# Optimization experiments

Measured on AMD Instinct MI355X. Metric: run time of the kernel, lower is better.

Reference implementation:

```python
import jax, jax.numpy as jnp
import numpy as np
from jax.ops import segment_sum, segment_max

N_NODES, N_EDGES, N_GRAPHS = 50000, 800000, 128
IN_C, HID, HEADS, CLIN = 64, 64, 4, 32


def gat_layer(x, W, a_s, a_d, b, src, dst, n):
    # GAT-style attention conv with concatenated heads (PyG GATConv math).
    H, C = a_s.shape
    h = (x @ W).reshape(-1, H, C)                      # [N,H,C]
    es = jnp.einsum('nhc,hc->nh', h, a_s)
    ed = jnp.einsum('nhc,hc->nh', h, a_d)
    e = jax.nn.leaky_relu(es[src] + ed[dst], 0.2)      # [E,H]
    m = segment_max(e, dst, num_segments=n)            # stable softmax over incoming edges
    e = jnp.exp(e - m[dst])
    denom = segment_sum(e, dst, num_segments=n)
    alpha = e / jnp.where(denom[dst] > 0, denom[dst], 1.0)
    out = segment_sum(h[src] * alpha[:, :, None], dst, num_segments=n)  # [N,H,C]
    return out.reshape(-1, H * C) + b


def label_prop(x, src, dst, n, num_layers=2, alpha=0.5):
    # PyG LabelPropagation: sym-normalized diffusion, residual mix, clamp to [0,1].
    deg = segment_sum(jnp.ones((src.shape[0],), x.dtype), dst, num_segments=n)
    dis = jnp.where(deg > 0, 1.0 / jnp.sqrt(jnp.maximum(deg, 1.0)), 0.0)
    norm = (dis[src] * dis[dst])[:, None]
    res = (1.0 - alpha) * x
    out = x
    for _ in range(num_layers):
        out = alpha * segment_sum(out[src] * norm, dst, num_segments=n) + res
        out = jnp.clip(out, 0.0, 1.0)
    return out


def mean_pool(x, batch, n_graphs):
    cnt = segment_sum(jnp.ones((x.shape[0],), x.dtype), batch, num_segments=n_graphs)
    s = segment_sum(x, batch, num_segments=n_graphs)
    return s / jnp.maximum(cnt, 1.0)[:, None]


def setup_inputs() -> dict:
    key = jax.random.key(0)
    ks = iter(jax.random.split(key, 32))
    def p(shape, fan_in):
        return jax.random.normal(next(ks), shape, jnp.float32) / np.sqrt(fan_in)
    d = {}
    d['x'] = jax.random.normal(next(ks), (N_NODES, IN_C), jnp.float32)
    d['edge_index'] = jax.random.randint(next(ks), (2, N_EDGES), 0, N_NODES)
    d['batch'] = jnp.sort(jax.random.randint(next(ks), (N_NODES,), 0, N_GRAPHS))
    d['clinical_data'] = jax.random.normal(next(ks), (N_GRAPHS, CLIN), jnp.float32)
    HC = HEADS * HID
    d['W1'] = p((IN_C, HC), IN_C); d['a1s'] = p((HEADS, HID), HID); d['a1d'] = p((HEADS, HID), HID); d['b1'] = jnp.zeros((HC,), jnp.float32)
    d['W2'] = p((HC, HC), HC); d['a2s'] = p((HEADS, HID), HID); d['a2d'] = p((HEADS, HID), HID); d['b2'] = jnp.zeros((HC,), jnp.float32)
    jk = IN_C + 2 * HC  # 576
    d['pp_w1'] = p((jk, 256), jk); d['pp_b1'] = jnp.zeros((256,), jnp.float32)
    d['pp_w2'] = p((256, 128), 256); d['pp_b2'] = jnp.zeros((128,), jnp.float32)
    d['cl_w1'] = p((CLIN, 64), CLIN); d['cl_b1'] = jnp.zeros((64,), jnp.float32)
    d['cl_w2'] = p((64, 32), 64); d['cl_b2'] = jnp.zeros((32,), jnp.float32)
    d['h_w1'] = p((160, 64), 160); d['h_b1'] = jnp.zeros((64,), jnp.float32)
    d['h_w2'] = p((64, 32), 64); d['h_b2'] = jnp.zeros((32,), jnp.float32)
    d['h_w3'] = p((32, 2), 32); d['h_b3'] = jnp.zeros((2,), jnp.float32)
    return d


def reference(x, edge_index, batch, clinical_data,
              W1, a1s, a1d, b1, W2, a2s, a2d, b2,
              pp_w1, pp_b1, pp_w2, pp_b2,
              cl_w1, cl_b1, cl_w2, cl_b2,
              h_w1, h_b1, h_w2, h_b2, h_w3, h_b3):
    src, dst = edge_index[0], edge_index[1]
    n = x.shape[0]
    h0 = x
    h1 = jax.nn.relu(gat_layer(h0, W1, a1s, a1d, b1, src, dst, n))
    h1 = label_prop(h1, src, dst, n)
    h2 = jax.nn.relu(gat_layer(h1, W2, a2s, a2d, b2, src, dst, n))
    h2 = label_prop(h2, src, dst, n)
    combined = jnp.concatenate([h0, h1, h2], axis=-1)           # [N, 576]
    g = mean_pool(combined, batch, N_GRAPHS)                    # [G, 576]
    v_graph = jax.nn.relu(g @ pp_w1 + pp_b1) @ pp_w2 + pp_b2    # [G, 128] (dropout = eval/no-op)
    v_clin = jax.nn.relu(clinical_data @ cl_w1 + cl_b1) @ cl_w2 + cl_b2  # [G, 32]
    z = jnp.concatenate([v_graph, v_clin], axis=-1)             # [G, 160]
    z = jax.nn.relu(z @ h_w1 + h_b1)
    z = jax.nn.relu(z @ h_w2 + h_b2)
    return z @ h_w3 + h_b3                                      # [G, 2]
```

## Files before the change

kernel.cpp:

```cpp
#include <hip/hip_runtime.h>

#define N_NODES 50000
#define N_EDGES 800000
#define N_GRAPHS 128
#define JK 576
#define CAP 192
#define NSB ((N_NODES + 255) / 256)
#define SLICE_U (N_NODES * 16)

typedef __attribute__((ext_vector_type(8))) short bf16x8;
typedef __attribute__((ext_vector_type(4))) float f32x4;

__device__ __forceinline__ unsigned f2_to_bf2(float a, float b) {
    unsigned ua = __float_as_uint(a), ub = __float_as_uint(b);
    ua = (ua + 0x7fffu + ((ua >> 16) & 1u)) >> 16;
    ub = (ub + 0x7fffu + ((ub >> 16) & 1u)) >> 16;
    return ua | (ub << 16);
}
__device__ __forceinline__ uint2 f4_to_bf4(float4 v) {
    return make_uint2(f2_to_bf2(v.x, v.y), f2_to_bf2(v.z, v.w));
}
__device__ __forceinline__ float4 bf4_to_f4(uint2 u) {
    float4 r;
    r.x = __uint_as_float(u.x << 16);
    r.y = __uint_as_float(u.x & 0xffff0000u);
    r.z = __uint_as_float(u.y << 16);
    r.w = __uint_as_float(u.y & 0xffff0000u);
    return r;
}

template<int BN, int KK, int SLA, int SLC>
__global__ __launch_bounds__(256)
void mfma_gemm(const unsigned short* __restrict__ Abf, int lda,
               const unsigned short* __restrict__ BT,
               unsigned* __restrict__ Cbf, int ldc,
               int M, const float* __restrict__ bias, int relu,
               int a_off, int b_off, int c_off) {
    __shared__ unsigned short As[64][32];
    __shared__ unsigned short Bs[BN][32];
    const int t = threadIdx.x;
    const int wav = t >> 6, lane = t & 63;
    const int quad = lane >> 4, l15 = lane & 15;
    const int m0 = blockIdx.x * 64;
    const int head = blockIdx.y;
    const unsigned short* Ab = Abf + (size_t)head * a_off;
    BT  += (size_t)head * b_off;
    const float* bptr = bias ? bias + (size_t)head * c_off : nullptr;
    unsigned* cbf = Cbf + (((size_t)head * c_off) >> 1);

    f32x4 acc[BN / 16];
#pragma unroll
    for (int i = 0; i < BN / 16; i++) acc[i] = (f32x4){0.f, 0.f, 0.f, 0.f};

    const int arow = t >> 2, aseg = t & 3;
    for (int k0 = 0; k0 < KK; k0 += 32) {
        uint4 av = make_uint4(0, 0, 0, 0);
        int gm = m0 + arow;
        if (gm < M) {
            if (SLA) {
                av = *(const uint4*)&Ab[(size_t)(k0 >> 5) * (N_NODES * 32) +
                                        (size_t)gm * 32 + aseg * 8];
            } else {
                av = *(const uint4*)&Ab[(size_t)gm * lda + k0 + aseg * 8];
            }
        }
        uint4 bv[BN == 256 ? 4 : 1];
        if (BN == 256) {
            const unsigned short* srcb = &BT[(size_t)t * KK + k0];
#pragma unroll
            for (int j = 0; j < 4; j++) bv[j] = *(const uint4*)&srcb[j * 8];
        } else {
            bv[0] = *(const uint4*)&BT[(size_t)arow * KK + k0 + aseg * 8];
        }
        __syncthreads();
        *(uint4*)&As[arow][aseg * 8] = av;
        if (BN == 256) {
#pragma unroll
            for (int j = 0; j < 4; j++) *(uint4*)&Bs[t][j * 8] = bv[j];
        } else {
            *(uint4*)&Bs[arow][aseg * 8] = bv[0];
        }
        __syncthreads();
        bf16x8 afrag = *(const bf16x8*)&As[wav * 16 + l15][quad * 8];
#pragma unroll
        for (int nt = 0; nt < BN / 16; nt++) {
            bf16x8 bfrag = *(const bf16x8*)&Bs[nt * 16 + l15][quad * 8];
            acc[nt] = __builtin_amdgcn_mfma_f32_16x16x32_bf16(afrag, bfrag, acc[nt], 0, 0, 0);
        }
    }
    int rbase = m0 + wav * 16 + quad * 4;
#pragma unroll
    for (int nt = 0; nt < BN / 16; nt++) {
        int col = nt * 16 + l15;
        float bb = bptr ? bptr[col] : 0.f;
#pragma unroll
        for (int r = 0; r < 4; r++) {
            int row = rbase + r;
            float v = acc[nt][r] + bb;
            if (relu) v = fmaxf(v, 0.f);
            float vp = __shfl_xor(v, 1);
            if (row < M && !(l15 & 1)) {
                if (SLC) {
                    int ch = head * c_off + col;
                    size_t a = (size_t)(ch >> 5) * SLICE_U + (size_t)row * 16 + ((ch & 31) >> 1);
                    Cbf[a] = f2_to_bf2(v, vp);
                } else {
                    cbf[((size_t)row * ldc + col) >> 1] = f2_to_bf2(v, vp);
                }
            }
        }
    }
}

__global__ void deg_kernel(const int* __restrict__ dst, int* __restrict__ deg,
                           const int* __restrict__ batch, int* __restrict__ gstart) {
    int t = blockIdx.x * blockDim.x + threadIdx.x;
    if (t < N_EDGES) {
        atomicAdd(&deg[dst[t]], 1);
    } else if (t < N_EDGES + N_NODES) {
        int n = t - N_EDGES;
        int b = batch[n];
        int prev = (n == 0) ? -1 : batch[n - 1];
        for (int g = prev + 1; g <= b; g++) gstart[g] = n;
        if (n == N_NODES - 1)
            for (int g = b + 1; g <= N_GRAPHS; g++) gstart[g] = N_NODES;
    }
}

#define S1 50000
#define S2 50256
#define S3 51280
#define S4 67664
#define S5 133200
#define S6 1733200
#define S7 (S6 + 131072)
__global__ void prep_misc(const int* __restrict__ deg, float* __restrict__ dis,
                          const float* __restrict__ W1, const float* __restrict__ a1s,
                          const float* __restrict__ a1d, float* __restrict__ wes1,
                          float* __restrict__ wed1,
                          const float* __restrict__ W2, const float* __restrict__ a2s,
                          const float* __restrict__ a2d, float* __restrict__ wes2,
                          float* __restrict__ wed2,
                          unsigned short* __restrict__ W1T, unsigned short* __restrict__ W2T,
                          const float* __restrict__ x, unsigned* __restrict__ xbf,
                          const int* __restrict__ gstart, float* __restrict__ psum) {
    int i = blockIdx.x * blockDim.x + threadIdx.x;
    if (i >= S7) return;
    if (i >= S6) {
        int t2 = i - S6;
        int g = t2 >> 10, rem = t2 & 1023;
        int q = rem >> 8, tid = rem & 255;
        int cp = tid & 63, np = tid >> 6;
        int n0 = gstart[g], n1 = gstart[g + 1];
        int len = n1 - n0;
        int ns = n0 + (len * q) / 4, ne = n0 + (len * (q + 1)) / 4;
        float s = 0.f;
        for (int n = ns + np; n < ne; n += 4) s += x[(size_t)n * 64 + cp];
        atomicAdd(&psum[g * JK + cp], s);
    } else if (i >= S5) {
        int j = i - S5;
        float2 v = *(const float2*)&x[(size_t)j * 2];
        xbf[j] = f2_to_bf2(v.x, v.y);
    } else if (i >= S4) {
        int t2 = i - S4;
        int n = t2 >> 8, c = t2 & 255;
        unsigned u = __float_as_uint(W2[(size_t)c * 256 + n]);
        u = (u + 0x7fffu + ((u >> 16) & 1u)) >> 16;
        W2T[t2] = (unsigned short)u;
    } else if (i >= S3) {
        int t2 = i - S3;
        int n = t2 >> 6, c = t2 & 63;
        unsigned u = __float_as_uint(W1[(size_t)c * 256 + n]);
        u = (u + 0x7fffu + ((u >> 16) & 1u)) >> 16;
        W1T[t2] = (unsigned short)u;
    } else if (i >= S2) {
        int t2 = i - S2;
        int c = t2 >> 2, h = t2 & 3;
        float se = 0.f, sd = 0.f;
        for (int j = 0; j < 64; j++) {
            float w = W2[(size_t)c * 256 + h * 64 + j];
            se += w * a2s[h * 64 + j];
            sd += w * a2d[h * 64 + j];
        }
        wes2[c * 4 + h] = se;
        wed2[c * 4 + h] = sd;
    } else if (i >= S1) {
        int t2 = i - S1;
        int c = t2 >> 2, h = t2 & 3;
        float se = 0.f, sd = 0.f;
        for (int j = 0; j < 64; j++) {
            float w = W1[(size_t)c * 256 + h * 64 + j];
            se += w * a1s[h * 64 + j];
            sd += w * a1d[h * 64 + j];
        }
        wes1[c * 4 + h] = se;
        wed1[c * 4 + h] = sd;
    } else {
        int d = deg[i];
        dis[i] = d > 0 ? rsqrtf((float)d) : 0.f;
    }
}
__global__ __launch_bounds__(256) void scan_bsum(const int* __restrict__ deg,
                                                 int* __restrict__ bsum) {
    __shared__ int sd[256];
    int n = blockIdx.x * 256 + threadIdx.x;
    sd[threadIdx.x] = (n < N_NODES) ? deg[n] : 0;
    __syncthreads();
    for (int o = 128; o > 0; o >>= 1) {
        if (threadIdx.x < o) sd[threadIdx.x] += sd[threadIdx.x + o];
        __syncthreads();
    }
    if (threadIdx.x == 0) bsum[blockIdx.x] = sd[0];
}
__global__ __launch_bounds__(256) void scan_bpre(const int* __restrict__ bsum,
                                                 int* __restrict__ bpre,
                                                 int* __restrict__ off_last) {
    __shared__ int sd[256];
    int t = threadIdx.x;
    int v = (t < NSB) ? bsum[t] : 0;
    sd[t] = v;
    __syncthreads();
    for (int o = 1; o < 256; o <<= 1) {
        int u = (t >= o) ? sd[t - o] : 0;
        __syncthreads();
        sd[t] += u;
        __syncthreads();
    }
    if (t < NSB) bpre[t] = sd[t] - v;
    if (t == 255) *off_last = sd[255];
}
__global__ __launch_bounds__(256) void scan_off(const int* __restrict__ deg,
                                                const int* __restrict__ bpre,
                                                int* __restrict__ off) {
    __shared__ int sd[256];
    int n = blockIdx.x * 256 + threadIdx.x;
    int t = threadIdx.x;
    int v = (n < N_NODES) ? deg[n] : 0;
    sd[t] = v;
    __syncthreads();
    for (int o = 1; o < 256; o <<= 1) {
        int u = (t >= o) ? sd[t - o] : 0;
        __syncthreads();
        sd[t] += u;
        __syncthreads();
    }
    if (n < N_NODES) off[n] = bpre[blockIdx.x] + sd[t] - v;
}
__global__ void csr_fill(const int* __restrict__ src, const int* __restrict__ dst,
                         const int* __restrict__ off, int* __restrict__ cursor,
                         int* __restrict__ csr_src, int2* __restrict__ csr_sw,
                         const float* __restrict__ dis) {
    int e = blockIdx.x * blockDim.x + threadIdx.x;
    if (e == 0) csr_sw[N_EDGES] = make_int2(0, 0);
    if (e >= N_EDGES) return;
    int s = src[e], d = dst[e];
    int pos = off[d] + atomicAdd(&cursor[d], 1);
    csr_src[pos] = s;
    float w = dis[s] * dis[d];
    csr_sw[pos] = make_int2(s, __float_as_int(w));
}

__global__ void esed_x(const float* __restrict__ X, const float* __restrict__ wes,
                       const float* __restrict__ wed, float* __restrict__ es,
                       float* __restrict__ ed) {
    int gid = blockIdx.x * blockDim.x + threadIdx.x;
    int n = gid >> 6, lane = threadIdx.x & 63;
    if (n >= N_NODES) return;
    float xv = X[(size_t)n * 64 + lane];
    float4 a = *(const float4*)&wes[lane * 4];
    float4 b = *(const float4*)&wed[lane * 4];
    float4 ps = make_float4(xv * a.x, xv * a.y, xv * a.z, xv * a.w);
    float4 pd = make_float4(xv * b.x, xv * b.y, xv * b.z, xv * b.w);
#pragma unroll
    for (int o = 1; o < 64; o <<= 1) {
        ps.x += __shfl_xor(ps.x, o); ps.y += __shfl_xor(ps.y, o);
        ps.z += __shfl_xor(ps.z, o); ps.w += __shfl_xor(ps.w, o);
        pd.x += __shfl_xor(pd.x, o); pd.y += __shfl_xor(pd.y, o);
        pd.z += __shfl_xor(pd.z, o); pd.w += __shfl_xor(pd.w, o);
    }
    if (lane == 0) {
        *(float4*)&es[n * 4] = ps;
        *(float4*)&ed[n * 4] = pd;
    }
}

__global__ void esed_h(const unsigned* __restrict__ Hsl, const float* __restrict__ wes,
                       const float* __restrict__ wed, float* __restrict__ es,
                       float* __restrict__ ed) {
    int gid = blockIdx.x * blockDim.x + threadIdx.x;
    int n = gid >> 6, lane = threadIdx.x & 63;
    if (n >= N_NODES) return;
    int sl = lane >> 3;
    uint2 u = *(const uint2*)&Hsl[(size_t)sl * SLICE_U + (size_t)n * 16 + (lane & 7) * 2];
    float4 vv = bf4_to_f4(u);
    float v0 = vv.x, v1 = vv.y, v2 = vv.z, v3 = vv.w;
    int ch0 = lane * 4;
    float4 a0 = *(const float4*)&wes[(ch0 + 0) * 4];
    float4 a1 = *(const float4*)&wes[(ch0 + 1) * 4];
    float4 a2 = *(const float4*)&wes[(ch0 + 2) * 4];
    float4 a3 = *(const float4*)&wes[(ch0 + 3) * 4];
    float4 b0 = *(const float4*)&wed[(ch0 + 0) * 4];
    float4 b1 = *(const float4*)&wed[(ch0 + 1) * 4];
    float4 b2 = *(const float4*)&wed[(ch0 + 2) * 4];
    float4 b3 = *(const float4*)&wed[(ch0 + 3) * 4];
    float4 ps, pd;
    ps.x = v0 * a0.x + v1 * a1.x + v2 * a2.x + v3 * a3.x;
    ps.y = v0 * a0.y + v1 * a1.y + v2 * a2.y + v3 * a3.y;
    ps.z = v0 * a0.z + v1 * a1.z + v2 * a2.z + v3 * a3.z;
    ps.w = v0 * a0.w + v1 * a1.w + v2 * a2.w + v3 * a3.w;
    pd.x = v0 * b0.x + v1 * b1.x + v2 * b2.x + v3 * b3.x;
    pd.y = v0 * b0.y + v1 * b1.y + v2 * b2.y + v3 * b3.y;
    pd.z = v0 * b0.z + v1 * b1.z + v2 * b2.z + v3 * b3.z;
    pd.w = v0 * b0.w + v1 * b1.w + v2 * b2.w + v3 * b3.w;
#pragma unroll
    for (int o = 1; o < 64; o <<= 1) {
        ps.x += __shfl_xor(ps.x, o); ps.y += __shfl_xor(ps.y, o);
        ps.z += __shfl_xor(ps.z, o); ps.w += __shfl_xor(ps.w, o);
        pd.x += __shfl_xor(pd.x, o); pd.y += __shfl_xor(pd.y, o);
        pd.z += __shfl_xor(pd.z, o); pd.w += __shfl_xor(pd.w, o);
    }
    if (lane == 0) {
        *(float4*)&es[n * 4] = ps;
        *(float4*)&ed[n * 4] = pd;
    }
}

__global__ __launch_bounds__(256)
void gat1_fused(const int* __restrict__ off, const int* __restrict__ csr_src,
                const float* __restrict__ es, const float* __restrict__ ed,
                const unsigned* __restrict__ xbf, unsigned* __restrict__ aggx_bf,
                float* __restrict__ alpha_fb) {
    __shared__ float elds[4][CAP * 4];
    __shared__ int   sidx[4][CAP];
    int wav = threadIdx.x >> 6, lane = threadIdx.x & 63;
    int n = blockIdx.x * 4 + wav;
    bool active = n < N_NODES;
    int p0 = 0, p1 = 0;
    float4 ed4 = make_float4(0.f, 0.f, 0.f, 0.f);
    if (active) { p0 = off[n]; p1 = off[n + 1]; ed4 = *(const float4*)&ed[n * 4]; }
    float4 sum = make_float4(0.f, 0.f, 0.f, 0.f);
    for (int p = p0 + lane; p < p1; p += 64) {
        int s = csr_src[p];
        float4 e4 = *(const float4*)&es[s * 4];
        e4.x += ed4.x; e4.y += ed4.y; e4.z += ed4.z; e4.w += ed4.w;
        e4.x = e4.x > 0.f ? e4.x : 0.2f * e4.x;
        e4.y = e4.y > 0.f ? e4.y : 0.2f * e4.y;
        e4.z = e4.z > 0.f ? e4.z : 0.2f * e4.z;
        e4.w = e4.w > 0.f ? e4.w : 0.2f * e4.w;
        e4.x = __expf(e4.x); e4.y = __expf(e4.y); e4.z = __expf(e4.z); e4.w = __expf(e4.w);
        int q = p - p0;
        if (q < CAP) { *(float4*)&elds[wav][q * 4] = e4; sidx[wav][q] = s; }
        else         *(float4*)&alpha_fb[(size_t)p * 4] = e4;
        sum.x += e4.x; sum.y += e4.y; sum.z += e4.z; sum.w += e4.w;
    }
#pragma unroll
    for (int o = 1; o < 64; o <<= 1) {
        sum.x += __shfl_xor(sum.x, o); sum.y += __shfl_xor(sum.y, o);
        sum.z += __shfl_xor(sum.z, o); sum.w += __shfl_xor(sum.w, o);
    }
    float4 rs;
    rs.x = sum.x > 0.f ? 1.f / sum.x : 0.f;
    rs.y = sum.y > 0.f ? 1.f / sum.y : 0.f;
    rs.z = sum.z > 0.f ? 1.f / sum.z : 0.f;
    rs.w = sum.w > 0.f ? 1.f / sum.w : 0.f;
    if (!active) return;
    int eg = lane >> 4, l15 = lane & 15;
    int deg = p1 - p0;
    float4 a0 = make_float4(0.f, 0.f, 0.f, 0.f);
    float4 a1 = a0, a2 = a0, a3 = a0;
    auto fetch = [&](int qq, float4& e4, float4& xv) {
        e4 = make_float4(0.f, 0.f, 0.f, 0.f);
        xv = e4;
        if (qq < deg) {
            int s;
            if (qq < CAP) { s = sidx[wav][qq]; e4 = *(const float4*)&elds[wav][qq * 4]; }
            else { s = csr_src[p0 + qq]; e4 = *(const float4*)&alpha_fb[(size_t)(p0 + qq) * 4]; }
            xv = bf4_to_f4(*(const uint2*)&xbf[(size_t)s * 32 + l15 * 2]);
        }
    };
    int q = eg;
    float4 eA, xA, eB, xB, eC, xC;
    fetch(q, eA, xA);
    fetch(q + 4, eB, xB);
    fetch(q + 8, eC, xC);
    while (q < deg) {
        float4 eD, xD;
        fetch(q + 12, eD, xD);
        a0.x += eA.x * xA.x; a0.y += eA.x * xA.y; a0.z += eA.x * xA.z; a0.w += eA.x * xA.w;
        a1.x += eA.y * xA.x; a1.y += eA.y * xA.y; a1.z += eA.y * xA.z; a1.w += eA.y * xA.w;
        a2.x += eA.z * xA.x; a2.y += eA.z * xA.y; a2.z += eA.z * xA.z; a2.w += eA.z * xA.w;
        a3.x += eA.w * xA.x; a3.y += eA.w * xA.y; a3.z += eA.w * xA.z; a3.w += eA.w * xA.w;
        eA = eB; xA = xB; eB = eC; xB = xC; eC = eD; xC = xD;
        q += 4;
    }
#pragma unroll
    for (int o = 16; o < 64; o <<= 1) {
        a0.x += __shfl_xor(a0.x, o); a0.y += __shfl_xor(a0.y, o);
        a0.z += __shfl_xor(a0.z, o); a0.w += __shfl_xor(a0.w, o);
        a1.x += __shfl_xor(a1.x, o); a1.y += __shfl_xor(a1.y, o);
        a1.z += __shfl_xor(a1.z, o); a1.w += __shfl_xor(a1.w, o);
        a2.x += __shfl_xor(a2.x, o); a2.y += __shfl_xor(a2.y, o);
        a2.z += __shfl_xor(a2.z, o); a2.w += __shfl_xor(a2.w, o);
        a3.x += __shfl_xor(a3.x, o); a3.y += __shfl_xor(a3.y, o);
        a3.z += __shfl_xor(a3.z, o); a3.w += __shfl_xor(a3.w, o);
    }
    if (eg == 0) {
        a0.x *= rs.x; a0.y *= rs.x; a0.z *= rs.x; a0.w *= rs.x;
        a1.x *= rs.y; a1.y *= rs.y; a1.z *= rs.y; a1.w *= rs.y;
        a2.x *= rs.z; a2.y *= rs.z; a2.z *= rs.z; a2.w *= rs.z;
        a3.x *= rs.w; a3.y *= rs.w; a3.z *= rs.w; a3.w *= rs.w;
        size_t b = (size_t)n * 128 + l15 * 2;
        *(uint2*)&aggx_bf[b +  0] = f4_to_bf4(a0);
        *(uint2*)&aggx_bf[b + 32] = f4_to_bf4(a1);
        *(uint2*)&aggx_bf[b + 64] = f4_to_bf4(a2);
        *(uint2*)&aggx_bf[b + 96] = f4_to_bf4(a3);
    }
}

__global__ __launch_bounds__(256)
void gat2_fused(const int* __restrict__ off, const int* __restrict__ csr_src,
                const float* __restrict__ es, const float* __restrict__ ed,
                const unsigned* __restrict__ H2bf, const float* __restrict__ bias,
                unsigned* __restrict__ outbf, float* __restrict__ alpha_fb) {
    __shared__ float elds[4][CAP * 4];
    __shared__ int   sidx[4][CAP];
    int wav = threadIdx.x >> 6, lane = threadIdx.x & 63;
    int n = blockIdx.x * 4 + wav;
    bool active = n < N_NODES;
    int p0 = 0, p1 = 0;
    float4 ed4 = make_float4(0.f, 0.f, 0.f, 0.f);
    if (active) { p0 = off[n]; p1 = off[n + 1]; ed4 = *(const float4*)&ed[n * 4]; }
    float4 sum = make_float4(0.f, 0.f, 0.f, 0.f);
    for (int p = p0 + lane; p < p1; p += 64) {
        int s = csr_src[p];
        float4 e4 = *(const float4*)&es[s * 4];
        e4.x += ed4.x; e4.y += ed4.y; e4.z += ed4.z; e4.w += ed4.w;
        e4.x = e4.x > 0.f ? e4.x : 0.2f * e4.x;
        e4.y = e4.y > 0.f ? e4.y : 0.2f * e4.y;
        e4.z = e4.z > 0.f ? e4.z : 0.2f * e4.z;
        e4.w = e4.w > 0.f ? e4.w : 0.2f * e4.w;
        e4.x = __expf(e4.x); e4.y = __expf(e4.y); e4.z = __expf(e4.z); e4.w = __expf(e4.w);
        int q = p - p0;
        if (q < CAP) { *(float4*)&elds[wav][q * 4] = e4; sidx[wav][q] = s; }
        else         *(float4*)&alpha_fb[(size_t)p * 4] = e4;
        sum.x += e4.x; sum.y += e4.y; sum.z += e4.z; sum.w += e4.w;
    }
#pragma unroll
    for (int o = 1; o < 64; o <<= 1) {
        sum.x += __shfl_xor(sum.x, o); sum.y += __shfl_xor(sum.y, o);
        sum.z += __shfl_xor(sum.z, o); sum.w += __shfl_xor(sum.w, o);
    }
    if (!active) return;
    int half = lane >> 5, l = lane & 31;
    int hh = l >> 3;
    float sh = (hh == 0) ? sum.x : (hh == 1) ? sum.y : (hh == 2) ? sum.z : sum.w;
    float rsh = sh > 0.f ? 1.f / sh : 0.f;
    int deg = p1 - p0;
    float acc[8];
#pragma unroll
    for (int j = 0; j < 8; j++) acc[j] = 0.f;
    auto fetch = [&](int qq, float& al, uint4& rr) {
        al = 0.f;
        rr = make_uint4(0, 0, 0, 0);
        if (qq < deg) {
            int s;
            if (qq < CAP) { s = sidx[wav][qq]; al = elds[wav][qq * 4 + hh]; }
            else { s = csr_src[p0 + qq]; al = alpha_fb[(size_t)(p0 + qq) * 4 + hh]; }
            rr = *(const uint4*)&H2bf[(size_t)s * 128 + l * 4];
        }
    };
    int q = half;
    float aA, aB, aC;
    uint4 rA, rB, rC;
    fetch(q, aA, rA);
    fetch(q + 2, aB, rB);
    fetch(q + 4, aC, rC);
    while (q < deg) {
        float aD; uint4 rD;
        fetch(q + 6, aD, rD);
        float4 f0 = bf4_to_f4(make_uint2(rA.x, rA.y));
        float4 f1 = bf4_to_f4(make_uint2(rA.z, rA.w));
        acc[0] += aA * f0.x; acc[1] += aA * f0.y; acc[2] += aA * f0.z; acc[3] += aA * f0.w;
        acc[4] += aA * f1.x; acc[5] += aA * f1.y; acc[6] += aA * f1.z; acc[7] += aA * f1.w;
        aA = aB; rA = rB; aB = aC; rB = rC; aC = aD; rC = rD;
        q += 2;
    }
#pragma unroll
    for (int j = 0; j < 8; j++) acc[j] += __shfl_xor(acc[j], 32);
    if (half == 0) {
        float4 b0 = *(const float4*)&bias[l * 8];
        float4 b1 = *(const float4*)&bias[l * 8 + 4];
        float4 o0, o1;
        o0.x = fmaxf(acc[0] * rsh + b0.x, 0.f);
        o0.y = fmaxf(acc[1] * rsh + b0.y, 0.f);
        o0.z = fmaxf(acc[2] * rsh + b0.z, 0.f);
        o0.w = fmaxf(acc[3] * rsh + b0.w, 0.f);
        o1.x = fmaxf(acc[4] * rsh + b1.x, 0.f);
        o1.y = fmaxf(acc[5] * rsh + b1.y, 0.f);
        o1.z = fmaxf(acc[6] * rsh + b1.z, 0.f);
        o1.w = fmaxf(acc[7] * rsh + b1.w, 0.f);
        uint2 w0 = f4_to_bf4(o0), w1 = f4_to_bf4(o1);
        uint4 w = make_uint4(w0.x, w0.y, w1.x, w1.y);
        size_t a = (size_t)(l >> 2) * SLICE_U + (size_t)n * 16 + (l & 3) * 4;
        *(uint4*)&outbf[a] = w;
    }
}

__global__ __launch_bounds__(256)
void lp_slice(const int* __restrict__ off, const int2* __restrict__ csr_sw,
              const unsigned* __restrict__ in_sl,
              const unsigned* __restrict__ res_sl, unsigned* __restrict__ out_sl) {
    int wav = threadIdx.x >> 6, lane = threadIdx.x & 63;
    int sl = blockIdx.x & 7, chunk = blockIdx.x >> 3;
    int n0 = chunk * 16 + wav * 4;
    int nsub = lane >> 4, e = (lane >> 2) & 3, seg = lane & 3;
    int n = n0 + nsub;
    int p0 = 0, p1 = 0;
    if (n < N_NODES) { p0 = off[n]; p1 = off[n + 1]; }
    int m = (p1 - p0 + 3) >> 2;
    m = max(m, __shfl_xor(m, 16));
    m = max(m, __shfl_xor(m, 32));
    const unsigned* base = in_sl + (size_t)sl * SLICE_U;
    float acc[8];
#pragma unroll
    for (int j = 0; j < 8; j++) acc[j] = 0.f;
    int p = p0 + e;
    if (m > 0) {
        int pe = (p < p1) ? p : N_EDGES;
        int2 sw = csr_sw[pe];
        for (int i = 0; i < m; i++) {
            p += 4;
            int pen = (p < p1 && i + 1 < m) ? p : N_EDGES;
            int2 swn = csr_sw[pen];
            float nw = __int_as_float(sw.y);
            uint4 rr = *(const uint4*)&base[((unsigned)sw.x << 4) + (seg << 2)];
            float4 f0 = bf4_to_f4(make_uint2(rr.x, rr.y));
            float4 f1 = bf4_to_f4(make_uint2(rr.z, rr.w));
            acc[0] += nw * f0.x; acc[1] += nw * f0.y;
            acc[2] += nw * f0.z; acc[3] += nw * f0.w;
            acc[4] += nw * f1.x; acc[5] += nw * f1.y;
            acc[6] += nw * f1.z; acc[7] += nw * f1.w;
            sw = swn;
        }
    }
#pragma unroll
    for (int o = 4; o <= 8; o <<= 1) {
#pragma unroll
        for (int j = 0; j < 8; j++) acc[j] += __shfl_xor(acc[j], o);
    }
    if (((lane & 12) == 0) && n < N_NODES) {
        size_t a = (size_t)sl * SLICE_U + (size_t)n * 16 + (seg << 2);
        uint4 rr = *(const uint4*)&res_sl[a];
        float4 r0 = bf4_to_f4(make_uint2(rr.x, rr.y));
        float4 r1 = bf4_to_f4(make_uint2(rr.z, rr.w));
        float4 o0, o1;
        o0.x = fminf(fmaxf(0.5f * acc[0] + 0.5f * r0.x, 0.f), 1.f);
        o0.y = fminf(fmaxf(0.5f * acc[1] + 0.5f * r0.y, 0.f), 1.f);
        o0.z = fminf(fmaxf(0.5f * acc[2] + 0.5f * r0.z, 0.f), 1.f);
        o0.w = fminf(fmaxf(0.5f * acc[3] + 0.5f * r0.w, 0.f), 1.f);
        o1.x = fminf(fmaxf(0.5f * acc[4] + 0.5f * r1.x, 0.f), 1.f);
        o1.y = fminf(fmaxf(0.5f * acc[5] + 0.5f * r1.y, 0.f), 1.f);
        o1.z = fminf(fmaxf(0.5f * acc[6] + 0.5f * r1.z, 0.f), 1.f);
        o1.w = fminf(fmaxf(0.5f * acc[7] + 0.5f * r1.w, 0.f), 1.f);
        uint2 w0 = f4_to_bf4(o0), w1 = f4_to_bf4(o1);
        *(uint4*)&out_sl[a] = make_uint4(w0.x, w0.y, w1.x, w1.y);
    }
}

__global__ void pool_bf(const unsigned* __restrict__ buf, const int* __restrict__ gstart,
                        float* __restrict__ psum, int colOff) {
    int g = blockIdx.x, q = blockIdx.y;
    int n0 = gstart[g], n1 = gstart[g + 1];
    int len = n1 - n0;
    int ns = n0 + (len * q) / 4, ne = n0 + (len * (q + 1)) / 4;
    int cp = threadIdx.x & 127;
    int np = threadIdx.x >> 7;
    size_t sbase = (size_t)(cp >> 4) * SLICE_U + (cp & 15);
    float s0 = 0.f, s1 = 0.f;
    for (int n = ns + np; n < ne; n += 2) {
        unsigned u = buf[sbase + (size_t)n * 16];
        s0 += __uint_as_float(u << 16);
        s1 += __uint_as_float(u & 0xffff0000u);
    }
    atomicAdd(&psum[g * JK + colOff + cp * 2 + 0], s0);
    atomicAdd(&psum[g * JK + colOff + cp * 2 + 1], s1);
}

__global__ __launch_bounds__(256)
void head_all(const float* __restrict__ psum, const int* __restrict__ gstart,
              const float* __restrict__ clin,
              const float* __restrict__ pp_w1, const float* __restrict__ pp_b1,
              const float* __restrict__ pp_w2, const float* __restrict__ pp_b2,
              const float* __restrict__ cl_w1, const float* __restrict__ cl_b1,
              const float* __restrict__ cl_w2, const float* __restrict__ cl_b2,
              const float* __restrict__ h_w1, const float* __restrict__ h_b1,
              const float* __restrict__ h_w2, const float* __restrict__ h_b2,
              const float* __restrict__ h_w3, const float* __restrict__ h_b3,
              float* __restrict__ out) {
    __shared__ float zin[JK];
    __shared__ float z1[256];
    __shared__ float zcl[32];
    __shared__ float zc[64];
    __shared__ float z[160];
    __shared__ float z3[64];
    __shared__ float z4[32];
    __shared__ float part[128];
    int g = blockIdx.x, t = threadIdx.x;
    int len = gstart[g + 1] - gstart[g];
    float inv = 1.f / (float)(len > 1 ? len : 1);
    for (int k = t; k < JK; k += 256) zin[k] = psum[g * JK + k] * inv;
    if (t < 32) zcl[t] = clin[g * 32 + t];
    __syncthreads();
    {
        float acc = pp_b1[t];
#pragma unroll 8
        for (int k = 0; k < JK; k++) acc += zin[k] * pp_w1[k * 256 + t];
        z1[t] = fmaxf(acc, 0.f);
    }
    __syncthreads();
    int m = t & 127, half = t >> 7;
    {
        float acc = 0.f;
        int k0 = half * 128;
#pragma unroll 8
        for (int k = k0; k < k0 + 128; k++) acc += z1[k] * pp_w2[k * 128 + m];
        if (half) part[m] = acc;
        __syncthreads();
        if (!half) z[m] = acc + part[m] + pp_b2[m];
    }
    if (t < 64) {
        float acc = cl_b1[t];
#pragma unroll
        for (int k = 0; k < 32; k++) acc += zcl[k] * cl_w1[k * 64 + t];
        zc[t] = fmaxf(acc, 0.f);
    }
    __syncthreads();
    if (t < 32) {
        float acc = cl_b2[t];
#pragma unroll
        for (int k = 0; k < 64; k++) acc += zc[k] * cl_w2[k * 32 + t];
        z[128 + t] = acc;
    }
    __syncthreads();
    if (t < 64) {
        float acc = h_b1[t];
#pragma unroll 8
        for (int k = 0; k < 160; k++) acc += z[k] * h_w1[k * 64 + t];
        z3[t] = fmaxf(acc, 0.f);
    }
    __syncthreads();
    if (t < 32) {
        float acc = h_b2[t];
#pragma unroll
        for (int k = 0; k < 64; k++) acc += z3[k] * h_w2[k * 32 + t];
        z4[t] = fmaxf(acc, 0.f);
    }
    __syncthreads();
    if (t < 2) {
        float acc = h_b3[t];
#pragma unroll
        for (int k = 0; k < 32; k++) acc += z4[k] * h_w3[k * 2 + t];
        out[g * 2 + t] = acc;
    }
}

extern "C" void kernel_launch(void* const* d_in, const int* in_sizes, int n_in,
                              void* d_out, int out_size, void* d_ws, size_t ws_size,
                              hipStream_t stream) {
    const float* x     = (const float*)d_in[0];
    const int*   ei    = (const int*)d_in[1];
    const int*   batch = (const int*)d_in[2];
    const float* clin  = (const float*)d_in[3];
    const float* W1  = (const float*)d_in[4];
    const float* a1s = (const float*)d_in[5];
    const float* a1d = (const float*)d_in[6];
    const float* b1  = (const float*)d_in[7];
    const float* W2  = (const float*)d_in[8];
    const float* a2s = (const float*)d_in[9];
    const float* a2d = (const float*)d_in[10];
    const float* b2  = (const float*)d_in[11];
    const float* pp_w1 = (const float*)d_in[12];
    const float* pp_b1 = (const float*)d_in[13];
    const float* pp_w2 = (const float*)d_in[14];
    const float* pp_b2 = (const float*)d_in[15];
    const float* cl_w1 = (const float*)d_in[16];
    const float* cl_b1 = (const float*)d_in[17];
    const float* cl_w2 = (const float*)d_in[18];
    const float* cl_b2 = (const float*)d_in[19];
    const float* h_w1  = (const float*)d_in[20];
    const float* h_b1  = (const float*)d_in[21];
    const float* h_w2  = (const float*)d_in[22];
    const float* h_b2  = (const float*)d_in[23];
    const float* h_w3  = (const float*)d_in[24];
    const float* h_b3  = (const float*)d_in[25];

    const int* src = ei;
    const int* dst = ei + N_EDGES;

    char* p = (char*)d_ws;
    auto carve = [&](size_t bytes) -> char* {
        char* r = p;
        p += (bytes + 255) & ~(size_t)255;
        return r;
    };
    const size_t NBH = (size_t)N_NODES * 256 * 2;
    unsigned* abf  = (unsigned*)carve(NBH);
    unsigned* bf1  = (unsigned*)carve(NBH);
    unsigned* bf2  = (unsigned*)carve(NBH);
    unsigned* bf3  = (unsigned*)carve(NBH);
    unsigned* xbf  = (unsigned*)carve((size_t)N_NODES * 32 * 4);
    float* alpha_fb  = (float*)carve((size_t)N_EDGES * 4 * 4);
    int*   csr_src   = (int*)carve((size_t)N_EDGES * 4);
    int2*  csr_sw    = (int2*)carve((size_t)(N_EDGES + 1) * 8);
    int*   off       = (int*)carve((size_t)(N_NODES + 1) * 4);
    int*   deg       = (int*)carve((size_t)N_NODES * 4);
    int*   cursor    = (int*)carve((size_t)N_NODES * 4);
    int*   bsum      = (int*)carve((size_t)NSB * 4);
    int*   bpre      = (int*)carve((size_t)NSB * 4);
    float* dis       = (float*)carve((size_t)N_NODES * 4);
    float* es        = (float*)carve((size_t)N_NODES * 4 * 4);
    float* ed        = (float*)carve((size_t)N_NODES * 4 * 4);
    float* wes1      = (float*)carve((size_t)64 * 4 * 4);
    float* wed1      = (float*)carve((size_t)64 * 4 * 4);
    float* wes2      = (float*)carve((size_t)256 * 4 * 4);
    float* wed2      = (float*)carve((size_t)256 * 4 * 4);
    unsigned short* W1T = (unsigned short*)carve((size_t)256 * 64 * 2);
    unsigned short* W2T = (unsigned short*)carve((size_t)256 * 256 * 2);
    int*   gstart    = (int*)carve((size_t)(N_GRAPHS + 1) * 4);
    float* psum      = (float*)carve((size_t)N_GRAPHS * JK * 4);

    const int TB = 256;
    const int gE     = (N_EDGES + TB - 1) / TB;
    const int gDeg   = (N_EDGES + N_NODES + TB - 1) / TB;
    const int gNwave = (N_NODES * 64 + TB - 1) / TB;
    const int gFuse  = (N_NODES + 3) / 4;
    const int gRow   = (N_NODES + 63) / 64;
    const int gPrep  = (S7 + TB - 1) / TB;
    const int gSlice = 8 * ((N_NODES + 15) / 16);

    hipMemsetAsync(deg, 0, (size_t)N_NODES * 4, stream);
    hipMemsetAsync(cursor, 0, (size_t)N_NODES * 4, stream);
    hipMemsetAsync(psum, 0, (size_t)N_GRAPHS * JK * 4, stream);
    deg_kernel<<<gDeg, TB, 0, stream>>>(dst, deg, batch, gstart);
    prep_misc<<<gPrep, TB, 0, stream>>>(deg, dis,
                                        W1, a1s, a1d, wes1, wed1,
                                        W2, a2s, a2d, wes2, wed2,
                                        W1T, W2T, x, xbf, gstart, psum);
    scan_bsum<<<NSB, 256, 0, stream>>>(deg, bsum);
    scan_bpre<<<1, 256, 0, stream>>>(bsum, bpre, &off[N_NODES]);
    scan_off<<<NSB, 256, 0, stream>>>(deg, bpre, off);
    csr_fill<<<gE, TB, 0, stream>>>(src, dst, off, cursor, csr_src, csr_sw, dis);

    esed_x<<<gNwave, TB, 0, stream>>>(x, wes1, wed1, es, ed);
    gat1_fused<<<gFuse, TB, 0, stream>>>(off, csr_src, es, ed, xbf, abf, alpha_fb);
    mfma_gemm<64, 64, 0, 1><<<dim3(gRow, 4), 256, 0, stream>>>(
        (const unsigned short*)abf, 256, W1T, bf1, 256, N_NODES, b1, 1,
        64, 64 * 64, 64);

    lp_slice<<<gSlice, TB, 0, stream>>>(off, csr_sw, bf1, bf1, bf2);
    lp_slice<<<gSlice, TB, 0, stream>>>(off, csr_sw, bf2, bf1, bf3);
    esed_h<<<gNwave, TB, 0, stream>>>(bf3, wes2, wed2, es, ed);

    pool_bf<<<dim3(N_GRAPHS, 4), TB, 0, stream>>>(bf3, gstart, psum, 64);

    mfma_gemm<256, 256, 1, 0><<<dim3(gRow, 1), 256, 0, stream>>>(
        (const unsigned short*)bf3, 256, W2T, bf1, 256, N_NODES, nullptr, 0,
        0, 0, 0);
    gat2_fused<<<gFuse, TB, 0, stream>>>(off, csr_src, es, ed, bf1, b2, bf2, alpha_fb);

    lp_slice<<<gSlice, TB, 0, stream>>>(off, csr_sw, bf2, bf2, bf1);
    lp_slice<<<gSlice, TB, 0, stream>>>(off, csr_sw, bf1, bf2, abf);

    pool_bf<<<dim3(N_GRAPHS, 4), TB, 0, stream>>>(abf, gstart, psum, 320);
    head_all<<<N_GRAPHS, 256, 0, stream>>>(psum, gstart, clin,
                                           pp_w1, pp_b1, pp_w2, pp_b2,
                                           cl_w1, cl_b1, cl_w2, cl_b2,
                                           h_w1, h_b1, h_w2, h_b2, h_w3, h_b3,
                                           (float*)d_out);
}
```

Before: 836.2 us.

## Pack CSR source and fp16 weight into 32 bits, deepen LP prefetch, stage GAT2 stores

After: 800.1 us. 4.3% less time.

```diff
diff --git a/kernel.cpp b/kernel.cpp
--- a/kernel.cpp
+++ b/kernel.cpp
@@ -1,4 +1,5 @@
 #include <hip/hip_runtime.h>
+#include <hip/hip_fp16.h>
 
 #define N_NODES 50000
 #define N_EDGES 800000
@@ -248,16 +249,17 @@
 }
 __global__ void csr_fill(const int* __restrict__ src, const int* __restrict__ dst,
                          const int* __restrict__ off, int* __restrict__ cursor,
-                         int* __restrict__ csr_src, int2* __restrict__ csr_sw,
+                         int* __restrict__ csr_src, unsigned* __restrict__ csr_sw,
                          const float* __restrict__ dis) {
     int e = blockIdx.x * blockDim.x + threadIdx.x;
-    if (e == 0) csr_sw[N_EDGES] = make_int2(0, 0);
+    if (e == 0) csr_sw[N_EDGES] = 0u;
     if (e >= N_EDGES) return;
     int s = src[e], d = dst[e];
     int pos = off[d] + atomicAdd(&cursor[d], 1);
     csr_src[pos] = s;
     float w = dis[s] * dis[d];
-    csr_sw[pos] = make_int2(s, __float_as_int(w));
+    unsigned hw = (unsigned)__half_as_ushort(__float2half(w));
+    csr_sw[pos] = (unsigned)s | (hw << 16);
 }
 
 __global__ void esed_x(const float* __restrict__ X, const float* __restrict__ wes,
@@ -424,12 +426,11 @@
                 unsigned* __restrict__ outbf, float* __restrict__ alpha_fb) {
     __shared__ float elds[4][CAP * 4];
     __shared__ int   sidx[4][CAP];
+    __shared__ unsigned stg[4][128];
     int wav = threadIdx.x >> 6, lane = threadIdx.x & 63;
     int n = blockIdx.x * 4 + wav;
-    bool active = n < N_NODES;
-    int p0 = 0, p1 = 0;
-    float4 ed4 = make_float4(0.f, 0.f, 0.f, 0.f);
-    if (active) { p0 = off[n]; p1 = off[n + 1]; ed4 = *(const float4*)&ed[n * 4]; }
+    int p0 = off[n], p1 = off[n + 1];
+    float4 ed4 = *(const float4*)&ed[n * 4];
     float4 sum = make_float4(0.f, 0.f, 0.f, 0.f);
     for (int p = p0 + lane; p < p1; p += 64) {
         int s = csr_src[p];
@@ -450,7 +451,6 @@
         sum.x += __shfl_xor(sum.x, o); sum.y += __shfl_xor(sum.y, o);
         sum.z += __shfl_xor(sum.z, o); sum.w += __shfl_xor(sum.w, o);
     }
-    if (!active) return;
     int half = lane >> 5, l = lane & 31;
     int hh = l >> 3;
     float sh = (hh == 0) ? sum.x : (hh == 1) ? sum.y : (hh == 2) ? sum.z : sum.w;
@@ -500,21 +500,29 @@
         o1.z = fmaxf(acc[6] * rsh + b1.z, 0.f);
         o1.w = fmaxf(acc[7] * rsh + b1.w, 0.f);
         uint2 w0 = f4_to_bf4(o0), w1 = f4_to_bf4(o1);
-        uint4 w = make_uint4(w0.x, w0.y, w1.x, w1.y);
-        size_t a = (size_t)(l >> 2) * SLICE_U + (size_t)n * 16 + (l & 3) * 4;
-        *(uint4*)&outbf[a] = w;
+        *(uint4*)&stg[wav][l * 4] = make_uint4(w0.x, w0.y, w1.x, w1.y);
+    }
+    __syncthreads();
+    {
+        int t = threadIdx.x;
+        int s = t >> 5;
+        int j = t & 31;
+        int node = j >> 3;
+        int dw = (j & 7) * 2;
+        uint2 v = make_uint2(stg[node][s * 16 + dw], stg[node][s * 16 + dw + 1]);
+        *(uint2*)&outbf[(size_t)s * SLICE_U + (size_t)(blockIdx.x * 4 + node) * 16 + dw] = v;
     }
 }
 
 __global__ __launch_bounds__(256)
-void lp_slice(const int* __restrict__ off, const int2* __restrict__ csr_sw,
+void lp_slice(const int* __restrict__ off, const unsigned* __restrict__ csr_sw,
               const unsigned* __restrict__ in_sl,
               const unsigned* __restrict__ res_sl, unsigned* __restrict__ out_sl) {
     int wav = threadIdx.x >> 6, lane = threadIdx.x & 63;
     int sl = blockIdx.x & 7, chunk = blockIdx.x >> 3;
-    int n0 = chunk * 16 + wav * 4;
+    int n0c = chunk * 16 + wav * 4;
     int nsub = lane >> 4, e = (lane >> 2) & 3, seg = lane & 3;
-    int n = n0 + nsub;
+    int n = n0c + nsub;
     int p0 = 0, p1 = 0;
     if (n < N_NODES) { p0 = off[n]; p1 = off[n + 1]; }
     int m = (p1 - p0 + 3) >> 2;
@@ -526,21 +534,25 @@
     for (int j = 0; j < 8; j++) acc[j] = 0.f;
     int p = p0 + e;
     if (m > 0) {
-        int pe = (p < p1) ? p : N_EDGES;
-        int2 sw = csr_sw[pe];
+        int peA = (p < p1) ? p : N_EDGES;
+        unsigned rA = csr_sw[peA];
+        int peB = (p + 4 < p1 && m > 1) ? p + 4 : N_EDGES;
+        unsigned rB = csr_sw[peB];
+        uint4 dA = *(const uint4*)&base[((rA & 0xffffu) << 4) + (seg << 2)];
         for (int i = 0; i < m; i++) {
-            p += 4;
-            int pen = (p < p1 && i + 1 < m) ? p : N_EDGES;
-            int2 swn = csr_sw[pen];
-            float nw = __int_as_float(sw.y);
-            uint4 rr = *(const uint4*)&base[((unsigned)sw.x << 4) + (seg << 2)];
-            float4 f0 = bf4_to_f4(make_uint2(rr.x, rr.y));
-            float4 f1 = bf4_to_f4(make_uint2(rr.z, rr.w));
+            int pn = p + 8;
+            int peC = (pn < p1 && i + 2 < m) ? pn : N_EDGES;
+            unsigned rC = csr_sw[peC];
+            uint4 dB = *(const uint4*)&base[((rB & 0xffffu) << 4) + (seg << 2)];
+            float nw = __half2float(__ushort_as_half((unsigned short)(rA >> 16)));
+            float4 f0 = bf4_to_f4(make_uint2(dA.x, dA.y));
+            float4 f1 = bf4_to_f4(make_uint2(dA.z, dA.w));
             acc[0] += nw * f0.x; acc[1] += nw * f0.y;
             acc[2] += nw * f0.z; acc[3] += nw * f0.w;
             acc[4] += nw * f1.x; acc[5] += nw * f1.y;
             acc[6] += nw * f1.z; acc[7] += nw * f1.w;
-            sw = swn;
+            rA = rB; rB = rC; dA = dB;
+            p += 4;
         }
     }
 #pragma unroll
@@ -711,7 +723,7 @@
     unsigned* xbf  = (unsigned*)carve((size_t)N_NODES * 32 * 4);
     float* alpha_fb  = (float*)carve((size_t)N_EDGES * 4 * 4);
     int*   csr_src   = (int*)carve((size_t)N_EDGES * 4);
-    int2*  csr_sw    = (int2*)carve((size_t)(N_EDGES + 1) * 8);
+    unsigned* csr_sw = (unsigned*)carve((size_t)(N_EDGES + 1) * 4);
     int*   off       = (int*)carve((size_t)(N_NODES + 1) * 4);
     int*   deg       = (int*)carve((size_t)N_NODES * 4);
     int*   cursor    = (int*)carve((size_t)N_NODES * 4);
```
